# Performance work log

Measured on AMD Instinct MI355X. Metric: run time of the kernel, lower is better.

## Reference

```python
import jax, jax.numpy as jnp
import numpy as np

EPS = 1e-6
NORM_FACTOR = 1000.0  # self.normalization_factor, aggregation 'sum'

# ---- Lorentz manifold (curvature -1, hyperboloid <x,x>_L = -1) ----

def _linner(x, y):
    # Lorentz inner product, keepdim on last axis
    return -x[..., :1] * y[..., :1] + jnp.sum(x[..., 1:] * y[..., 1:], axis=-1, keepdims=True)

def _proj_tan0(u):
    return jnp.concatenate([jnp.zeros_like(u[..., :1]), u[..., 1:]], axis=-1)

def _expmap0(u):
    sp = u[..., 1:]
    n = jnp.sqrt(jnp.clip(jnp.sum(sp * sp, axis=-1, keepdims=True), EPS))
    return jnp.concatenate([jnp.cosh(n), jnp.sinh(n) / n * sp], axis=-1)

def _logmap0(x):
    x0 = jnp.clip(x[..., :1], 1.0 + EPS)
    d = jnp.arccosh(x0)
    sp = x[..., 1:] * (d / jnp.sqrt(x0 * x0 - 1.0))
    return jnp.concatenate([jnp.zeros_like(x0), sp], axis=-1)

def _dist(x, y):
    return jnp.arccosh(jnp.clip(-_linner(x, y), 1.0 + EPS))

def _logmap(x, y):
    alpha = jnp.clip(-_linner(x, y), 1.0 + EPS)
    u = y - alpha * x                      # y + <x,y>_L x
    return jnp.arccosh(alpha) * u / jnp.sqrt(alpha * alpha - 1.0)

def _expmap(x, u):
    n = jnp.sqrt(jnp.clip(_linner(u, u), EPS))
    return jnp.cosh(n) * x + jnp.sinh(n) / n * u

def _proju(x, u):
    return u + _linner(x, u) * x

def _transp0(y, v):
    # parallel transport from origin o=(1,0,...,0) to y
    coef = _linner(y, v) / (1.0 + y[..., :1])
    oy = jnp.concatenate([y[..., :1] + 1.0, y[..., 1:]], axis=-1)
    return v + coef * oy

def _layernorm(x, g, b, eps=1e-5):
    m = jnp.mean(x, axis=-1, keepdims=True)
    v = jnp.mean((x - m) ** 2, axis=-1, keepdims=True)
    return (x - m) / jnp.sqrt(v + eps) * g + b


def setup_inputs() -> dict:
    N, E, D, ED = 10000, 320000, 128, 2
    key = jax.random.key(0)
    ks = jax.random.split(key, 10)
    # nodes on the hyperboloid: expmap0 of a small tangent vector
    h_tan = 0.02 * jax.random.normal(ks[0], (N, D), dtype=jnp.float32)
    h = _expmap0(_proj_tan0(h_tan))
    edge_attr = jax.random.normal(ks[1], (E, ED), dtype=jnp.float32)
    row = jax.random.randint(ks[2], (E,), 0, N, dtype=jnp.int32)
    col = jax.random.randint(ks[3], (E,), 0, N, dtype=jnp.int32)
    node_mask = jnp.ones((N, 1), dtype=jnp.float32)
    edge_mask = jnp.ones((E, 1), dtype=jnp.float32)
    s = 1.0 / np.sqrt(D)
    W = s * jax.random.normal(ks[4], (D, D), dtype=jnp.float32)
    bias = 0.0 * jax.random.normal(ks[5], (1, D), dtype=jnp.float32)  # init.constant_(bias, 0)
    att_in = 2 * D + ED + 1  # x_row, x_col, edge_attr + geodesic
    att_w1 = (1.0 / np.sqrt(att_in)) * jax.random.normal(ks[6], (att_in, D), dtype=jnp.float32)
    att_b1 = jnp.zeros((D,), dtype=jnp.float32)
    att_w2 = s * jax.random.normal(ks[7], (D, 1), dtype=jnp.float32)
    att_b2 = jnp.zeros((1,), dtype=jnp.float32)
    ln_gamma = jnp.ones((D - 1,), dtype=jnp.float32)
    ln_beta = jnp.zeros((D - 1,), dtype=jnp.float32)
    return {"h": h, "edge_attr": edge_attr, "row": row, "col": col,
            "node_mask": node_mask, "edge_mask": edge_mask, "W": W, "bias": bias,
            "att_w1": att_w1, "att_b1": att_b1, "att_w2": att_w2, "att_b2": att_b2,
            "ln_gamma": ln_gamma, "ln_beta": ln_beta}


def reference(h, edge_attr, row, col, node_mask, edge_mask, W, bias,
              att_w1, att_b1, att_w2, att_b2, ln_gamma, ln_beta):
    N = h.shape[0]
    # ---- HypLinear ----
    xt = _logmap0(h) @ W                  # Linear(in,out,bias=False)
    x = _expmap0(_proj_tan0(xt))
    b = _transp0(x, _proj_tan0(bias))
    x = _expmap(x, b)
    # ---- HypAgg ----
    x_tan = _logmap0(x)
    xr, xc = x[row], x[col]
    geo = _dist(xr, xc)                   # [E,1]
    att_in = jnp.concatenate([x_tan[row], x_tan[col], edge_attr, geo], axis=-1)
    hid = jax.nn.silu(att_in @ att_w1 + att_b1)
    att = jax.nn.sigmoid(hid @ att_w2 + att_b2) * edge_mask   # [E,1]
    loc = _logmap(xr, xc)                 # [E,D]
    agg = jax.ops.segment_sum(loc * att, row, num_segments=N) / NORM_FACTOR
    x = _expmap(x, _proju(x, agg))
    # ---- HNorm (Lorentz: LN on spatial components only) ----
    ht = _logmap0(x)
    sp = _layernorm(ht[..., 1:], ln_gamma, ln_beta)
    x = _expmap0(jnp.concatenate([ht[..., :1], sp], axis=-1))
    # ---- HypAct (manifold_out = Lorentz as well) ----
    xt = _proj_tan0(jax.nn.silu(_logmap0(x)))
    return _expmap0(xt)
```

## Files before the change

kernel.cpp:

```cpp
#include <hip/hip_runtime.h>
#include <hip/hip_fp16.h>
#include <math.h>

#define D 128
#define NPB 8
#define EPS1 (1.0f + 1e-6f)

__device__ __forceinline__ float dpp_rsum16(float v) {
    v += __int_as_float(__builtin_amdgcn_update_dpp(
        0, __float_as_int(v), 0x121, 0xf, 0xf, true));
    v += __int_as_float(__builtin_amdgcn_update_dpp(
        0, __float_as_int(v), 0x122, 0xf, 0xf, true));
    v += __int_as_float(__builtin_amdgcn_update_dpp(
        0, __float_as_int(v), 0x124, 0xf, 0xf, true));
    v += __int_as_float(__builtin_amdgcn_update_dpp(
        0, __float_as_int(v), 0x128, 0xf, 0xf, true));
    return v;
}

__device__ __forceinline__ float facosh(float a) {
    return __logf(a + sqrtf(fmaxf(a * a - 1.0f, 0.0f)));
}

__device__ __forceinline__ void unpack8(const float4& a, const float4& b,
                                        float* d) {
    d[0] = a.x; d[1] = a.y; d[2] = a.z; d[3] = a.w;
    d[4] = b.x; d[5] = b.y; d[6] = b.z; d[7] = b.w;
}

__device__ __forceinline__ void unpackh8(const float4& v, float* d) {
    const __half2* p = (const __half2*)&v;
#pragma unroll
    for (int t = 0; t < 4; t++) {
        float2 f = __half22float2(p[t]);
        d[2 * t] = f.x;
        d[2 * t + 1] = f.y;
    }
}

__device__ __forceinline__ void bsumH2(float* v, float (*wred)[2], int lane,
                                       int wid, int kp) {
    __syncthreads();
#pragma unroll
    for (int o = 32; o; o >>= 1)
#pragma unroll
        for (int nl = 0; nl < 2; nl++) v[nl] += __shfl_xor(v[nl], o, 64);
    if (lane == 0)
#pragma unroll
        for (int nl = 0; nl < 2; nl++) wred[wid][nl] = v[nl];
    __syncthreads();
#pragma unroll
    for (int nl = 0; nl < 2; nl++)
        v[nl] = wred[2 * kp][nl] + wred[2 * kp + 1][nl];
}

__global__ __launch_bounds__(512) void node_pre8(
    const float* __restrict__ h, const float* __restrict__ W,
    const float* __restrict__ bias, const float* __restrict__ att_w1,
    const float* __restrict__ att_b1, float* __restrict__ Xrow,
    __half* __restrict__ XQh, float* __restrict__ P_out,
    const int* __restrict__ row, int* __restrict__ cnt, int N, int E) {
    int i0 = blockIdx.x * NPB;
    int tid = threadIdx.x;
    int j = tid & 127, kp = tid >> 7;
    int lane = tid & 63, wid = tid >> 6;
    int nbase = kp * 2;
    __shared__ __align__(16) float t8[NPB][D];
    __shared__ float psumP[4][NPB][D];
    __shared__ float psumQ[4][NPB][D];
    __shared__ float wred[8][2];

    float hj[2];
#pragma unroll
    for (int nl = 0; nl < 2; nl++) {
        int gi = i0 + nbase + nl;
        hj[nl] = (gi < N) ? h[(size_t)gi * D + j] : 0.0f;
        t8[nbase + nl][j] = hj[nl];
    }
    __syncthreads();
    float tj[2];
#pragma unroll
    for (int nl = 0; nl < 2; nl++) {
        float h0 = fmaxf(t8[nbase + nl][0], EPS1);
        float fac = facosh(h0) * rsqrtf(h0 * h0 - 1.0f);
        tj[nl] = (j == 0) ? 0.0f : hj[nl] * fac;
    }
    __syncthreads();
#pragma unroll
    for (int nl = 0; nl < 2; nl++) t8[nbase + nl][j] = tj[nl];
    __syncthreads();

    float xtp[NPB];
#pragma unroll
    for (int n = 0; n < NPB; n++) xtp[n] = 0.0f;
    int kbeg = kp * 32;
    for (int k0 = kbeg; k0 < kbeg + 32; k0 += 4) {
        float w0 = W[(k0 + 0) * D + j], w1 = W[(k0 + 1) * D + j];
        float w2 = W[(k0 + 2) * D + j], w3 = W[(k0 + 3) * D + j];
#pragma unroll
        for (int n = 0; n < NPB; n++) {
            float4 tv = *(const float4*)&t8[n][k0];
            xtp[n] = fmaf(tv.x, w0,
                          fmaf(tv.y, w1, fmaf(tv.z, w2, fmaf(tv.w, w3, xtp[n]))));
        }
    }
#pragma unroll
    for (int n = 0; n < NPB; n++) psumP[kp][n][j] = xtp[n];
    __syncthreads();
    float xt[2];
#pragma unroll
    for (int nl = 0; nl < 2; nl++) {
        int n = nbase + nl;
        xt[nl] = (j == 0) ? 0.0f
                          : (psumP[0][n][j] + psumP[1][n][j] + psumP[2][n][j] +
                             psumP[3][n][j]);
    }

    float v2[2];
#pragma unroll
    for (int nl = 0; nl < 2; nl++) v2[nl] = xt[nl] * xt[nl];
    bsumH2(v2, wred, lane, wid, kp);
    float xj[2];
#pragma unroll
    for (int nl = 0; nl < 2; nl++) {
        float nn = sqrtf(fmaxf(v2[nl], 1e-6f));
        float e = __expf(nn), ei = __fdividef(1.0f, e);
        float ch = 0.5f * (e + ei), sh = 0.5f * (e - ei);
        xj[nl] = (j == 0) ? ch : __fdividef(sh, nn) * xt[nl];
    }

    float vj = (j == 0) ? 0.0f : bias[j];
#pragma unroll
    for (int nl = 0; nl < 2; nl++) v2[nl] = xj[nl] * vj;
    bsumH2(v2, wred, lane, wid, kp);
    __syncthreads();
#pragma unroll
    for (int nl = 0; nl < 2; nl++) t8[nbase + nl][j] = xj[nl];
    __syncthreads();
    float bj[2];
#pragma unroll
    for (int nl = 0; nl < 2; nl++) {
        float X0 = t8[nbase + nl][0];
        float coef = __fdividef(v2[nl], 1.0f + X0);
        bj[nl] = vj + coef * ((j == 0) ? (X0 + 1.0f) : xj[nl]);
    }
#pragma unroll
    for (int nl = 0; nl < 2; nl++)
        v2[nl] = (j == 0) ? -bj[nl] * bj[nl] : bj[nl] * bj[nl];
    bsumH2(v2, wred, lane, wid, kp);
    float xnj[2];
#pragma unroll
    for (int nl = 0; nl < 2; nl++) {
        float nb = sqrtf(fmaxf(v2[nl], 1e-6f));
        float e = __expf(nb), ei = __fdividef(1.0f, e);
        float ch = 0.5f * (e + ei), sh = 0.5f * (e - ei);
        xnj[nl] = ch * xj[nl] + __fdividef(sh, nb) * bj[nl];
        int gi = i0 + nbase + nl;
        if (gi < N) {
            Xrow[(size_t)gi * D + j] = xnj[nl];
            XQh[(size_t)gi * 256 + j] = __float2half(xnj[nl]);
        }
    }

    __syncthreads();
#pragma unroll
    for (int nl = 0; nl < 2; nl++) t8[nbase + nl][j] = xnj[nl];
    __syncthreads();
    float xtj[2];
#pragma unroll
    for (int nl = 0; nl < 2; nl++) {
        float Y0 = fmaxf(t8[nbase + nl][0], EPS1);
        float f = facosh(Y0) * rsqrtf(Y0 * Y0 - 1.0f);
        xtj[nl] = (j == 0) ? 0.0f : xnj[nl] * f;
    }
    __syncthreads();
#pragma unroll
    for (int nl = 0; nl < 2; nl++) t8[nbase + nl][j] = xtj[nl];
    __syncthreads();

    float pp[NPB], qq[NPB];
#pragma unroll
    for (int n = 0; n < NPB; n++) {
        pp[n] = 0.0f;
        qq[n] = 0.0f;
    }
    for (int k0 = kbeg; k0 < kbeg + 32; k0 += 4) {
        float a0 = att_w1[(k0 + 0) * D + j], a1 = att_w1[(k0 + 1) * D + j];
        float a2 = att_w1[(k0 + 2) * D + j], a3 = att_w1[(k0 + 3) * D + j];
        float c0 = att_w1[(D + k0 + 0) * D + j], c1 = att_w1[(D + k0 + 1) * D + j];
        float c2 = att_w1[(D + k0 + 2) * D + j], c3 = att_w1[(D + k0 + 3) * D + j];
#pragma unroll
        for (int n = 0; n < NPB; n++) {
            float4 tv = *(const float4*)&t8[n][k0];
            pp[n] = fmaf(tv.x, a0,
                         fmaf(tv.y, a1, fmaf(tv.z, a2, fmaf(tv.w, a3, pp[n]))));
            qq[n] = fmaf(tv.x, c0,
                         fmaf(tv.y, c1, fmaf(tv.z, c2, fmaf(tv.w, c3, qq[n]))));
        }
    }
#pragma unroll
    for (int n = 0; n < NPB; n++) {
        psumP[kp][n][j] = pp[n];
        psumQ[kp][n][j] = qq[n];
    }
    __syncthreads();
    float b1 = att_b1[j];
#pragma unroll
    for (int nl = 0; nl < 2; nl++) {
        int n = nbase + nl;
        int gi = i0 + n;
        if (gi < N) {
            P_out[(size_t)gi * D + j] = psumP[0][n][j] + psumP[1][n][j] +
                                        psumP[2][n][j] + psumP[3][n][j] + b1;
            float q = psumQ[0][n][j] + psumQ[1][n][j] + psumQ[2][n][j] +
                      psumQ[3][n][j];
            XQh[(size_t)gi * 256 + 128 + j] = __float2half(q);
        }
    }

    int gtid = blockIdx.x * 512 + tid;
    int tot = gridDim.x * 512;
    for (int e2 = gtid; e2 < E; e2 += tot) atomicAdd(&cnt[row[e2]], 1);
}

__global__ __launch_bounds__(1024) void scan_kernel(const int* __restrict__ cnt,
                                                    int* __restrict__ off,
                                                    int* __restrict__ cursor,
                                                    int N) {
    __shared__ int wt[16];
    int tid = threadIdx.x, lane = tid & 63, wid = tid >> 6;
    int PER = (N + 1023) >> 10;
    int basei = tid * PER;
    int loc[16];
    int tsum = 0;
#pragma unroll 4
    for (int r = 0; r < PER; r++) {
        int idx = basei + r;
        int v = (idx < N) ? cnt[idx] : 0;
        loc[r] = tsum;
        tsum += v;
    }
    int inc = tsum;
#pragma unroll
    for (int o = 1; o < 64; o <<= 1) {
        int t = __shfl_up(inc, o, 64);
        if (lane >= o) inc += t;
    }
    if (lane == 63) wt[wid] = inc;
    __syncthreads();
    if (tid < 16) {
        int w = wt[tid];
#pragma unroll
        for (int o = 1; o < 16; o <<= 1) {
            int t = __shfl_up(w, o, 64);
            if ((tid & 15) >= o) w += t;
        }
        wt[tid] = w;
    }
    __syncthreads();
    int wbase = (wid == 0) ? 0 : wt[wid - 1];
    int texcl = wbase + inc - tsum;
    for (int r = 0; r < PER; r++) {
        int idx = basei + r;
        if (idx < N) {
            int o = texcl + loc[r];
            off[idx] = o;
            cursor[idx] = o;
        }
    }
}

__global__ void scatter_kernel(const int* __restrict__ row,
                               const int* __restrict__ col,
                               const float* __restrict__ edge_attr,
                               const float* __restrict__ edge_mask,
                               int* __restrict__ cursor,
                               float4* __restrict__ rec, int E) {
    const float2* ea2 = (const float2*)edge_attr;
    for (int e = blockIdx.x * blockDim.x + threadIdx.x; e < E;
         e += gridDim.x * blockDim.x) {
        int r = row[e];
        int pos = atomicAdd(&cursor[r], 1);
        float2 a = ea2[e];
        rec[pos] = make_float4(__int_as_float(col[e]), a.x, a.y, edge_mask[e]);
    }
}

__global__ __launch_bounds__(256) void edge_agg(
    const float* __restrict__ Xrow, const float* __restrict__ P,
    const __half* __restrict__ XQh, const float4* __restrict__ rec,
    const int* __restrict__ off, const int* __restrict__ cnt,
    const float* __restrict__ w1c, const float* __restrict__ att_w2,
    const float* __restrict__ att_b2, const float* __restrict__ gamma,
    const float* __restrict__ beta, float* __restrict__ out, int N) {
    int tid = threadIdx.x, lane = tid & 63;
    int sub = lane & 15, grp = lane >> 4;
    int i = blockIdx.x * 4 + (tid >> 6);
    bool valid = i < N;
    i = min(i, N - 1);
    int j8 = sub * 8, f4 = sub * 2;

    const float4* w4 = (const float4*)w1c;
    const float4* aw4 = (const float4*)att_w2;
    const float4* xr4 = (const float4*)(Xrow + (size_t)i * D);
    const float4* pr4 = (const float4*)(P + (size_t)i * D);
    float xr[8], pr[8], wa[8], wb[8], wg[8], w2v[8];
    unpack8(xr4[f4], xr4[f4 + 1], xr);
    unpack8(pr4[f4], pr4[f4 + 1], pr);
    unpack8(w4[f4], w4[f4 + 1], wa);
    unpack8(w4[32 + f4], w4[32 + f4 + 1], wb);
    unpack8(w4[64 + f4], w4[64 + f4 + 1], wg);
    unpack8(aw4[f4], aw4[f4 + 1], w2v);
    float b2 = att_b2[0];
    float xr0s = (sub == 0) ? -xr[0] : xr[0];

    float acc[8];
#pragma unroll
    for (int u = 0; u < 8; u++) acc[u] = 0.0f;

    int s = off[i], m = valid ? cnt[i] : 0;
    int clen = (m + 3) >> 2;
    int k0 = grp * clen;
    int len = min(m, k0 + clen) - k0;

    auto compute = [&](const float4& rc, const float4& g0, const float4& g1,
                       bool act) {
        float xc[8], qc[8];
        unpackh8(g0, xc);
        unpackh8(g1, qc);
        float lin = xr0s * xc[0];
#pragma unroll
        for (int u = 1; u < 8; u++) lin = fmaf(xr[u], xc[u], lin);
        lin = dpp_rsum16(lin);
        float alpha = fmaxf(-lin, EPS1);
        float a2m = fmaxf(fmaf(alpha, alpha, -1.0f), 1e-12f);
        float rden = rsqrtf(a2m);
        float geo = __logf(fmaf(a2m, rden, alpha));
        float lp = 0.0f;
#pragma unroll
        for (int u = 0; u < 8; u++) {
            float hv = pr[u] + qc[u] +
                       fmaf(rc.y, wa[u], fmaf(rc.z, wb[u], geo * wg[u]));
            float sig = __fdividef(1.0f, 1.0f + __expf(-hv));
            lp = fmaf(hv * sig, w2v[u], lp);
        }
        lp = dpp_rsum16(lp);
        float w = act ? rc.w : 0.0f;
        float att = w * __fdividef(1.0f, 1.0f + __expf(-(lp + b2)));
        float scale = att * geo * rden * 1e-3f;
#pragma unroll
        for (int u = 0; u < 8; u++)
            acc[u] = fmaf(scale, fmaf(-alpha, xr[u], xc[u]), acc[u]);
    };

    float4 rcA = make_float4(__int_as_float(0), 0.0f, 0.0f, 0.0f), rcB;
    if (len > 0) rcA = rec[s + k0];
    const float4* pA =
        (const float4*)(XQh + (size_t)__float_as_int(rcA.x) * 256);
    float4 gA0 = pA[sub], gA1 = pA[16 + sub];
    float4 gB0, gB1;

    for (int t = 0; t < clen; t += 2) {
        rcB = rcA;
        if (t + 1 < len) rcB = rec[s + k0 + t + 1];
        const float4* pB =
            (const float4*)(XQh + (size_t)__float_as_int(rcB.x) * 256);
        gB0 = pB[sub];
        gB1 = pB[16 + sub];
        compute(rcA, gA0, gA1, t < len);
        rcA = rcB;
        if (t + 2 < len) rcA = rec[s + k0 + t + 2];
        const float4* pN =
            (const float4*)(XQh + (size_t)__float_as_int(rcA.x) * 256);
        gA0 = pN[sub];
        gA1 = pN[16 + sub];
        compute(rcB, gB0, gB1, t + 1 < len);
    }

#pragma unroll
    for (int u = 0; u < 8; u++) {
        acc[u] += __shfl_xor(acc[u], 16, 64);
        acc[u] += __shfl_xor(acc[u], 32, 64);
    }

    float lxa_p = (sub == 0) ? -xr[0] * acc[0] : xr[0] * acc[0];
#pragma unroll
    for (int u = 1; u < 8; u++) lxa_p = fmaf(xr[u], acc[u], lxa_p);
    float lxa = dpp_rsum16(lxa_p);
    float uj[8];
#pragma unroll
    for (int u = 0; u < 8; u++) uj[u] = fmaf(lxa, xr[u], acc[u]);
    float luu_p = (sub == 0) ? -uj[0] * uj[0] : uj[0] * uj[0];
#pragma unroll
    for (int u = 1; u < 8; u++) luu_p = fmaf(uj[u], uj[u], luu_p);
    float luu = dpp_rsum16(luu_p);
    float nn = sqrtf(fmaxf(luu, 1e-6f));
    float e = __expf(nn), ei = __fdividef(1.0f, e);
    float ch = 0.5f * (e + ei), shv = __fdividef(0.5f * (e - ei), nn);
    float xn[8];
#pragma unroll
    for (int u = 0; u < 8; u++) xn[u] = ch * xr[u] + shv * uj[u];
    float X0 = __shfl(xn[0], lane & 48, 64);
    X0 = fmaxf(X0, EPS1);
    float fc = facosh(X0) * rsqrtf(X0 * X0 - 1.0f);
    float ht[8];
#pragma unroll
    for (int u = 0; u < 8; u++) ht[u] = xn[u] * fc;
    if (sub == 0) ht[0] = 0.0f;
    float mp = 0.0f;
#pragma unroll
    for (int u = 0; u < 8; u++) mp += ht[u];
    float mean = dpp_rsum16(mp) * (1.0f / 127.0f);
    float diff[8];
#pragma unroll
    for (int u = 0; u < 8; u++) diff[u] = ht[u] - mean;
    if (sub == 0) diff[0] = 0.0f;
    float vp = 0.0f;
#pragma unroll
    for (int u = 0; u < 8; u++) vp = fmaf(diff[u], diff[u], vp);
    float var = dpp_rsum16(vp) * (1.0f / 127.0f);
    float rstd = rsqrtf(var + 1e-5f);
    float sp[8];
#pragma unroll
    for (int u = 0; u < 8; u++) {
        int j = j8 + u;
        float g = (j > 0) ? gamma[j - 1] : 0.0f;
        float bt = (j > 0) ? beta[j - 1] : 0.0f;
        sp[u] = fmaf(diff[u] * rstd, g, bt);
    }
    if (sub == 0) sp[0] = 0.0f;
    float n2p = 0.0f;
#pragma unroll
    for (int u = 0; u < 8; u++) n2p = fmaf(sp[u], sp[u], n2p);
    float n2 = sqrtf(fmaxf(dpp_rsum16(n2p), 1e-6f));
    e = __expf(n2);
    ei = __fdividef(1.0f, e);
    float y0 = 0.5f * (e + ei), sh2 = __fdividef(0.5f * (e - ei), n2);
    float yj[8];
#pragma unroll
    for (int u = 0; u < 8; u++) yj[u] = sh2 * sp[u];
    if (sub == 0) yj[0] = y0;
    float y0c = fmaxf(y0, EPS1);
    float f3 = facosh(y0c) * rsqrtf(y0c * y0c - 1.0f);
    float sj[8];
#pragma unroll
    for (int u = 0; u < 8; u++) {
        float lj = yj[u] * f3;
        sj[u] = __fdividef(lj, 1.0f + __expf(-lj));
    }
    if (sub == 0) sj[0] = 0.0f;
    float n3p = 0.0f;
#pragma unroll
    for (int u = 0; u < 8; u++) n3p = fmaf(sj[u], sj[u], n3p);
    float n3 = sqrtf(fmaxf(dpp_rsum16(n3p), 1e-6f));
    e = __expf(n3);
    ei = __fdividef(1.0f, e);
    float o0 = 0.5f * (e + ei), sh3 = __fdividef(0.5f * (e - ei), n3);
    float ov[8];
#pragma unroll
    for (int u = 0; u < 8; u++) ov[u] = sh3 * sj[u];
    if (sub == 0) ov[0] = o0;
    if (valid && grp == 0) {
        float4* o4 = (float4*)(out + (size_t)i * D);
        o4[f4] = make_float4(ov[0], ov[1], ov[2], ov[3]);
        o4[f4 + 1] = make_float4(ov[4], ov[5], ov[6], ov[7]);
    }
}

extern "C" void kernel_launch(void* const* d_in, const int* in_sizes, int n_in,
                              void* d_out, int out_size, void* d_ws,
                              size_t ws_size, hipStream_t stream) {
    const float* h = (const float*)d_in[0];
    const float* edge_attr = (const float*)d_in[1];
    const int* row = (const int*)d_in[2];
    const int* col = (const int*)d_in[3];
    const float* edge_mask = (const float*)d_in[5];
    const float* W = (const float*)d_in[6];
    const float* bias = (const float*)d_in[7];
    const float* att_w1 = (const float*)d_in[8];
    const float* att_b1 = (const float*)d_in[9];
    const float* att_w2 = (const float*)d_in[10];
    const float* att_b2 = (const float*)d_in[11];
    const float* ln_g = (const float*)d_in[12];
    const float* ln_b = (const float*)d_in[13];

    int N = in_sizes[0] / D;
    int E = in_sizes[2];

    float* Xrow = (float*)d_ws;
    float* Pbuf = Xrow + (size_t)N * D;
    __half* XQh = (__half*)(Pbuf + (size_t)N * D);
    float4* rec = (float4*)(XQh + (size_t)N * 256);
    int* cnt = (int*)(rec + E);
    int* off = cnt + N;
    int* cur = off + N;

    hipMemsetAsync(cnt, 0, N * sizeof(int), stream);
    node_pre8<<<(N + NPB - 1) / NPB, 512, 0, stream>>>(
        h, W, bias, att_w1, att_b1, Xrow, XQh, Pbuf, row, cnt, N, E);
    scan_kernel<<<1, 1024, 0, stream>>>(cnt, off, cur, N);
    scatter_kernel<<<640, 256, 0, stream>>>(row, col, edge_attr, edge_mask,
                                            cur, rec, E);
    edge_agg<<<(N + 3) / 4, 256, 0, stream>>>(Xrow, Pbuf, XQh, rec, off, cnt,
                                              att_w1 + 256 * D, att_w2, att_b2,
                                              ln_g, ln_b, (float*)d_out, N);
}
```

Measured before the change: 145.1 us.

## Split node edges across two waves, shuffle-broadcast records, move node epilogue to separate kernel

Each node's edge list is now split across two wavefronts (8 sub-groups instead of 4). Each 16-lane group loads up to 16 edge records at once and broadcasts them with shuffles, and gathers run as a 3-deep software pipeline. Per-wave partial sums go to a workspace buffer, and a new node_post kernel combines them and runs the expmap/norm/activation epilogue with all lanes active. This aims to raise parallelism and latency hiding for the gather-bound edge loop, at the cost of an extra kernel launch and a round trip through global memory for the partials.

Measured after the change: 146.4 us. No clear change (+0.9%).

```diff
diff --git a/kernel.cpp b/kernel.cpp
--- a/kernel.cpp
+++ b/kernel.cpp
@@ -291,14 +291,14 @@
     const __half* __restrict__ XQh, const float4* __restrict__ rec,
     const int* __restrict__ off, const int* __restrict__ cnt,
     const float* __restrict__ w1c, const float* __restrict__ att_w2,
-    const float* __restrict__ att_b2, const float* __restrict__ gamma,
-    const float* __restrict__ beta, float* __restrict__ out, int N) {
-    int tid = threadIdx.x, lane = tid & 63;
-    int sub = lane & 15, grp = lane >> 4;
-    int i = blockIdx.x * 4 + (tid >> 6);
+    const float* __restrict__ att_b2, float* __restrict__ aggP, int N) {
+    int tid = threadIdx.x, lane = tid & 63, wid = tid >> 6;
+    int sub = lane & 15, grp = lane >> 4, gb = lane & 48;
+    int i = blockIdx.x * 2 + (wid >> 1);
+    int w = wid & 1;
     bool valid = i < N;
     i = min(i, N - 1);
-    int j8 = sub * 8, f4 = sub * 2;
+    int f4 = sub * 2;
 
     const float4* w4 = (const float4*)w1c;
     const float4* aw4 = (const float4*)att_w2;
@@ -319,12 +319,17 @@
     for (int u = 0; u < 8; u++) acc[u] = 0.0f;
 
     int s = off[i], m = valid ? cnt[i] : 0;
-    int clen = (m + 3) >> 2;
-    int k0 = grp * clen;
-    int len = min(m, k0 + clen) - k0;
-
-    auto compute = [&](const float4& rc, const float4& g0, const float4& g1,
-                       bool act) {
+    int clen = (m + 7) >> 3;
+    int base = (w * 4 + grp) * clen;
+    int len = min(m - base, clen);
+    if (len < 0) len = 0;
+
+    float4 rp = make_float4(__int_as_float(0), 0.0f, 0.0f, 0.0f);
+    if (sub < len) rp = rec[s + base + sub];
+    int colp = __float_as_int(rp.x);
+
+    auto computeE = [&](float eay, float eaz, float msk, bool act,
+                        const float4& g0, const float4& g1) {
         float xc[8], qc[8];
         unpackh8(g0, xc);
         unpackh8(g1, qc);
@@ -340,41 +345,51 @@
 #pragma unroll
         for (int u = 0; u < 8; u++) {
             float hv = pr[u] + qc[u] +
-                       fmaf(rc.y, wa[u], fmaf(rc.z, wb[u], geo * wg[u]));
+                       fmaf(eay, wa[u], fmaf(eaz, wb[u], geo * wg[u]));
             float sig = __fdividef(1.0f, 1.0f + __expf(-hv));
             lp = fmaf(hv * sig, w2v[u], lp);
         }
         lp = dpp_rsum16(lp);
-        float w = act ? rc.w : 0.0f;
-        float att = w * __fdividef(1.0f, 1.0f + __expf(-(lp + b2)));
+        float wq = act ? msk : 0.0f;
+        float att = wq * __fdividef(1.0f, 1.0f + __expf(-(lp + b2)));
         float scale = att * geo * rden * 1e-3f;
 #pragma unroll
         for (int u = 0; u < 8; u++)
             acc[u] = fmaf(scale, fmaf(-alpha, xr[u], xc[u]), acc[u]);
     };
 
-    float4 rcA = make_float4(__int_as_float(0), 0.0f, 0.0f, 0.0f), rcB;
-    if (len > 0) rcA = rec[s + k0];
-    const float4* pA =
-        (const float4*)(XQh + (size_t)__float_as_int(rcA.x) * 256);
-    float4 gA0 = pA[sub], gA1 = pA[16 + sub];
-    float4 gB0, gB1;
-
-    for (int t = 0; t < clen; t += 2) {
-        rcB = rcA;
-        if (t + 1 < len) rcB = rec[s + k0 + t + 1];
-        const float4* pB =
-            (const float4*)(XQh + (size_t)__float_as_int(rcB.x) * 256);
-        gB0 = pB[sub];
-        gB1 = pB[16 + sub];
-        compute(rcA, gA0, gA1, t < len);
-        rcA = rcB;
-        if (t + 2 < len) rcA = rec[s + k0 + t + 2];
-        const float4* pN =
-            (const float4*)(XQh + (size_t)__float_as_int(rcA.x) * 256);
-        gA0 = pN[sub];
-        gA1 = pN[16 + sub];
-        compute(rcB, gB0, gB1, t + 1 < len);
+    int tmax = min(clen, 16);
+
+    {
+        int c0 = __shfl(colp, gb | 0, 64);
+        const float4* p0 = (const float4*)(XQh + (size_t)c0 * 256);
+        float4 gA0 = p0[sub], gA1 = p0[16 + sub];
+        int c1 = __shfl(colp, gb | 1, 64);
+        const float4* p1 = (const float4*)(XQh + (size_t)c1 * 256);
+        float4 gB0 = p1[sub], gB1 = p1[16 + sub];
+        float4 gC0, gC1;
+
+        for (int t = 0; t < tmax; ++t) {
+            int cn = __shfl(colp, gb | ((t + 2) & 15), 64);
+            const float4* pn = (const float4*)(XQh + (size_t)cn * 256);
+            gC0 = pn[sub];
+            gC1 = pn[16 + sub];
+            float eay = __shfl(rp.y, gb | t, 64);
+            float eaz = __shfl(rp.z, gb | t, 64);
+            float msk = __shfl(rp.w, gb | t, 64);
+            computeE(eay, eaz, msk, t < len, gA0, gA1);
+            gA0 = gB0; gA1 = gB1;
+            gB0 = gC0; gB1 = gC1;
+        }
+    }
+    for (int t = 16; t < clen; ++t) {
+        bool act = t < len;
+        float4 rc = make_float4(__int_as_float(0), 0.0f, 0.0f, 0.0f);
+        if (act) rc = rec[s + base + t];
+        const float4* pt =
+            (const float4*)(XQh + (size_t)__float_as_int(rc.x) * 256);
+        float4 g0 = pt[sub], g1 = pt[16 + sub];
+        computeE(rc.y, rc.z, rc.w, act, g0, g1);
     }
 
 #pragma unroll
@@ -382,6 +397,33 @@
         acc[u] += __shfl_xor(acc[u], 16, 64);
         acc[u] += __shfl_xor(acc[u], 32, 64);
     }
+    if (valid && grp == 0) {
+        float4* a4 = (float4*)(aggP + (size_t)(2 * i + w) * D);
+        a4[f4] = make_float4(acc[0], acc[1], acc[2], acc[3]);
+        a4[f4 + 1] = make_float4(acc[4], acc[5], acc[6], acc[7]);
+    }
+}
+
+__global__ __launch_bounds__(256) void node_post(
+    const float* __restrict__ Xrow, const float* __restrict__ aggP,
+    const float* __restrict__ gamma, const float* __restrict__ beta,
+    float* __restrict__ out, int N) {
+    int tid = threadIdx.x, lane = tid & 63;
+    int sub = lane & 15;
+    int i = blockIdx.x * 16 + (tid >> 4);
+    bool valid = i < N;
+    i = min(i, N - 1);
+    int j8 = sub * 8, f4 = sub * 2;
+
+    const float4* xr4 = (const float4*)(Xrow + (size_t)i * D);
+    const float4* a4a = (const float4*)(aggP + (size_t)(2 * i) * D);
+    const float4* a4b = (const float4*)(aggP + (size_t)(2 * i + 1) * D);
+    float xr[8], p0[8], p1[8], acc[8];
+    unpack8(xr4[f4], xr4[f4 + 1], xr);
+    unpack8(a4a[f4], a4a[f4 + 1], p0);
+    unpack8(a4b[f4], a4b[f4 + 1], p1);
+#pragma unroll
+    for (int u = 0; u < 8; u++) acc[u] = p0[u] + p1[u];
 
     float lxa_p = (sub == 0) ? -xr[0] * acc[0] : xr[0] * acc[0];
 #pragma unroll
@@ -460,7 +502,7 @@
 #pragma unroll
     for (int u = 0; u < 8; u++) ov[u] = sh3 * sj[u];
     if (sub == 0) ov[0] = o0;
-    if (valid && grp == 0) {
+    if (valid) {
         float4* o4 = (float4*)(out + (size_t)i * D);
         o4[f4] = make_float4(ov[0], ov[1], ov[2], ov[3]);
         o4[f4 + 1] = make_float4(ov[4], ov[5], ov[6], ov[7]);
@@ -494,6 +536,7 @@
     int* cnt = (int*)(rec + E);
     int* off = cnt + N;
     int* cur = off + N;
+    float* aggP = (float*)(cur + N);
 
     hipMemsetAsync(cnt, 0, N * sizeof(int), stream);
     node_pre8<<<(N + NPB - 1) / NPB, 512, 0, stream>>>(
@@ -501,7 +544,9 @@
     scan_kernel<<<1, 1024, 0, stream>>>(cnt, off, cur, N);
     scatter_kernel<<<640, 256, 0, stream>>>(row, col, edge_attr, edge_mask,
                                             cur, rec, E);
-    edge_agg<<<(N + 3) / 4, 256, 0, stream>>>(Xrow, Pbuf, XQh, rec, off, cnt,
-                                              att_w1 + 256 * D, att_w2, att_b2,
-                                              ln_g, ln_b, (float*)d_out, N);
-}
+    edge_agg<<<(N + 1) / 2, 256, 0, stream>>>(Xrow, Pbuf, XQh, rec, off, cnt,
+                                              att_w1 + 256 * D, att_w2,
+                                              att_b2, aggP, N);
+    node_post<<<(N + 15) / 16, 256, 0, stream>>>(Xrow, aggP, ln_g, ln_b,
+                                                 (float*)d_out, N);
+}
```
